# Performance work log

Measured on AMD Instinct MI355X. Metric: run time of the kernel, lower is better.

The kernel has to match this reference:

```python
import jax, jax.numpy as jnp
import numpy as np

D_MODEL = 1024
NUM_HEADS = 16
HEAD_DIM = D_MODEL // NUM_HEADS
B, S = 4, 2048


def setup_inputs() -> dict:
    key = jax.random.key(0)
    ks = jax.random.split(key, 6)
    scale = 1.0 / np.sqrt(D_MODEL)
    return {
        "q": jax.random.normal(ks[0], (B, S, D_MODEL), dtype=jnp.float32),
        "k": jax.random.normal(ks[1], (B, S, D_MODEL), dtype=jnp.float32),
        "v": jax.random.normal(ks[2], (B, S, D_MODEL), dtype=jnp.float32),
        "Wq": jax.random.normal(ks[3], (D_MODEL, D_MODEL), dtype=jnp.float32) * scale,
        "Wk": jax.random.normal(ks[4], (D_MODEL, D_MODEL), dtype=jnp.float32) * scale,
        "Wv": jax.random.normal(ks[5], (D_MODEL, D_MODEL), dtype=jnp.float32) * scale,
    }


def reference(q, k, v, Wq, Wk, Wv):
    b, s, d = q.shape
    # nn.Linear(bias=False): x @ W.T
    qp = jnp.einsum('bsd,ed->bse', q, Wq)
    kp = jnp.einsum('bsd,ed->bse', k, Wk)
    vp = jnp.einsum('bsd,ed->bse', v, Wv)
    # split heads -> (B, H, S, Dh)
    qh = qp.reshape(b, s, NUM_HEADS, HEAD_DIM).transpose(0, 2, 1, 3)
    kh = kp.reshape(b, s, NUM_HEADS, HEAD_DIM).transpose(0, 2, 1, 3)
    vh = vp.reshape(b, s, NUM_HEADS, HEAD_DIM).transpose(0, 2, 1, 3)
    scores = jnp.einsum('bhqd,bhkd->bhqk', qh, kh) / jnp.sqrt(jnp.float32(HEAD_DIM))
    attn = jax.nn.softmax(scores, axis=-1)
    att = jnp.einsum('bhqk,bhkd->bhqd', attn, vh)
    # NOTE: faithful to the source, which does a raw .view (no head transpose back)
    return att.reshape(b, s, d)
```

## Files before the change

kernel.cpp:

```cpp
#include <hip/hip_runtime.h>
#include <hip/hip_bf16.h>
#include <stdint.h>

#define D_MODEL 1024
#define NHEAD   16
#define HDIM    64
#define BATCH   4
#define SEQ     2048
#define NTOK    (BATCH*SEQ)

typedef __bf16          b16x8 __attribute__((ext_vector_type(8)));
typedef unsigned short  u16x8 __attribute__((ext_vector_type(8)));
typedef unsigned short  u16x4 __attribute__((ext_vector_type(4)));
typedef float           f32x4 __attribute__((ext_vector_type(4)));

__device__ __forceinline__ unsigned short f2b(float f) {
  union { float f; uint32_t u; } c; c.f = f;
  return (unsigned short)((c.u + 0x7FFFu + ((c.u >> 16) & 1u)) >> 16);
}

__device__ __forceinline__ uint32_t cvtpk(float lo, float hi) {
  uint32_t r;
  asm("v_cvt_pk_bf16_f32 %0, %1, %2" : "=v"(r) : "v"(lo), "v"(hi));
  return r;
}

__device__ __forceinline__ b16x8 cv8(f32x4 a, f32x4 b) {
  b16x8 r;
#pragma unroll
  for (int i = 0; i < 4; i++) { r[i] = (__bf16)a[i]; r[i + 4] = (__bf16)b[i]; }
  return r;
}

__device__ __forceinline__ void glds16(const void* g, void* l) {
  __builtin_amdgcn_global_load_lds(
      (const __attribute__((address_space(1))) unsigned int*)g,
      (__attribute__((address_space(3))) unsigned int*)l, 16, 0, 0);
}

__global__ __launch_bounds__(256, 8)
void wpack_kernel(const float* __restrict__ Wq, const float* __restrict__ Wk,
                  const float* __restrict__ Wv, unsigned short* __restrict__ wsp) {
  int bid = blockIdx.x;
  int which = bid >> 8;
  int tn = (bid >> 5) & 7;
  int kt = bid & 31;
  const float* W = (which == 0) ? Wq : ((which == 1) ? Wk : Wv);
  int t = threadIdx.x;
  int r = t >> 1;
  int sw0 = (t & 1) * 2;
  char* dst = (char*)wsp + (size_t)bid * 8192 + t * 32;
  const float* src = W + (size_t)(tn * 128 + r) * D_MODEL + kt * 32;
#pragma unroll
  for (int i = 0; i < 2; i++) {
    int s = (sw0 + i) ^ ((r >> 1) & 3);
    f32x4 a = *(const f32x4*)(src + s * 8);
    f32x4 b = *(const f32x4*)(src + s * 8 + 4);
    u16x8 pk;
#pragma unroll
    for (int j = 0; j < 4; j++) { pk[j] = f2b(a[j]); pk[j + 4] = f2b(b[j]); }
    *(u16x8*)(dst + i * 16) = pk;
  }
}

__global__ __launch_bounds__(256, 3)
void proj_gemm_f32a(const float* __restrict__ q, const float* __restrict__ k,
                    const float* __restrict__ v, const unsigned short* __restrict__ wsp,
                    unsigned short* __restrict__ qp, unsigned short* __restrict__ kp,
                    unsigned short* __restrict__ vt) {
  __shared__ __align__(16) char lds[2][24576];

  int bid = blockIdx.x;
  int swz = (bid & 7) * 192 + (bid >> 3);
  int which = swz >> 9;
  int rr = swz & 511;
  int tm = rr >> 3, tn = rr & 7;

  const float* X = (which == 0) ? q : ((which == 1) ? k : v);
  const char* Bpack = (const char*)wsp + (size_t)((which * 8 + tn) * 32) * 8192;

  int tid  = threadIdx.x;
  int lane = tid & 63;
  int w    = tid >> 6;
  int g    = lane >> 4;
  int c    = lane & 15;
  int chi  = c & 7;
  int wr   = (w >> 1) * 64;
  int wc   = (w & 1) * 64;

  f32x4 acc[4][4];
#pragma unroll
  for (int m = 0; m < 4; m++)
#pragma unroll
    for (int n = 0; n < 4; n++) acc[m][n] = (f32x4){0.f, 0.f, 0.f, 0.f};

  int arowl = lane >> 3;
  int aswz  = ((lane & 7) ^ arowl) << 4;
  const char* Asrc = (const char*)(X + (size_t)(tm * 128 + w * 32 + arowl) * D_MODEL) + aswz;
  const char* Bsrc = Bpack + w * 2048 + lane * 16;

  int aoff0 = (wr + c) * 128 + ((2 * g    ^ chi) << 4);
  int aoff1 = (wr + c) * 128 + (((2*g+1) ^ chi) << 4);
  int rboff = 16384 + (wc + c) * 64 + ((g ^ ((c >> 1) & 3)) << 4);

#pragma unroll
  for (int i = 0; i < 4; i++)
    glds16(Asrc + (size_t)i * 8 * D_MODEL * 4, lds[0] + w * 4096 + i * 1024);
  glds16(Bsrc,        lds[0] + 16384 + w * 2048);
  glds16(Bsrc + 1024, lds[0] + 16384 + w * 2048 + 1024);

  for (int kt = 0; kt < 32; kt++) {
    __syncthreads();
    if (kt < 31) {
      char* nb = lds[(kt + 1) & 1];
#pragma unroll
      for (int i = 0; i < 4; i++)
        glds16(Asrc + (size_t)i * 8 * D_MODEL * 4 + (kt + 1) * 128, nb + w * 4096 + i * 1024);
      glds16(Bsrc + (size_t)(kt + 1) * 8192,        nb + 16384 + w * 2048);
      glds16(Bsrc + (size_t)(kt + 1) * 8192 + 1024, nb + 16384 + w * 2048 + 1024);
    }
    const char* buf = lds[kt & 1];
    b16x8 af[4];
    u16x8 bf[4];
#pragma unroll
    for (int m = 0; m < 4; m++) {
      f32x4 a0 = *(const f32x4*)(buf + aoff0 + m * 2048);
      f32x4 a1 = *(const f32x4*)(buf + aoff1 + m * 2048);
      af[m] = cv8(a0, a1);
    }
#pragma unroll
    for (int n = 0; n < 4; n++)
      bf[n] = *(const u16x8*)(buf + rboff + n * 1024);
#pragma unroll
    for (int m = 0; m < 4; m++)
#pragma unroll
      for (int n = 0; n < 4; n++)
        acc[m][n] = __builtin_amdgcn_mfma_f32_16x16x32_bf16(
            af[m], __builtin_bit_cast(b16x8, bf[n]), acc[m][n], 0, 0, 0);
  }

  int cbase = tn * 128 + wc;
  int rbase = tm * 128 + wr;
  if (which < 2) {
    unsigned short* OutP = (which == 0) ? qp : kp;
    float scale = (which == 0) ? 0.18033688f : 1.0f;
#pragma unroll
    for (int m = 0; m < 4; m++)
#pragma unroll
      for (int n = 0; n < 4; n++) {
        int e = cbase + n * 16 + c;
        int h = e >> 6, dh = e & 63;
#pragma unroll
        for (int j = 0; j < 4; j++) {
          int i = rbase + m * 16 + g * 4 + j;
          int b = i >> 11, s = i & 2047;
          OutP[(((size_t)(b * NHEAD + h)) * SEQ + s) * HDIM + dh] =
              f2b(acc[m][n][j] * scale);
        }
      }
  } else {
#pragma unroll
    for (int m = 0; m < 4; m++)
#pragma unroll
      for (int n = 0; n < 4; n++) {
        int e = cbase + n * 16 + c;
        int h = e >> 6, dh = e & 63;
        int i0 = rbase + m * 16 + g * 4;
        int b = i0 >> 11, s0 = i0 & 2047;
        u16x4 pk;
#pragma unroll
        for (int j = 0; j < 4; j++) pk[j] = f2b(acc[m][n][j]);
        *(u16x4*)&vt[(((size_t)(b * NHEAD + h)) * HDIM + dh) * SEQ + s0] = pk;
      }
  }
}

#define KVB 64
__global__ __launch_bounds__(256, 4)
void attn_kernel(const unsigned short* __restrict__ qp,
                 const unsigned short* __restrict__ kp,
                 const unsigned short* __restrict__ vt,
                 float* __restrict__ out) {
  __shared__ __align__(16) char lds[2][16384];

  int bid = blockIdx.x;
  int swz = (bid & 7) * 128 + (bid >> 3);
  int bh = swz >> 4;
  int qb = swz & 15;

  int tid  = threadIdx.x;
  int lane = tid & 63;
  int w    = tid >> 6;
  int g    = lane >> 4;
  int c    = lane & 15;
  int chi  = c & 7;

  const unsigned short* Kg = kp + (size_t)bh * SEQ * HDIM;
  const unsigned short* Vg = vt + (size_t)bh * HDIM * SEQ;

  int q0 = qb * 128 + w * 32;
  u16x8 qf[2][2];
#pragma unroll
  for (int qg = 0; qg < 2; qg++)
#pragma unroll
    for (int h = 0; h < 2; h++)
      qf[qg][h] = *(const u16x8*)&qp[((size_t)bh * SEQ + q0 + qg * 16 + c) * HDIM + h * 32 + g * 8];

  f32x4 o[4][2];
#pragma unroll
  for (int d = 0; d < 4; d++)
#pragma unroll
    for (int qg = 0; qg < 2; qg++) o[d][qg] = (f32x4){0.f, 0.f, 0.f, 0.f};
  f32x4 lacc[2];
  lacc[0] = (f32x4){0.f, 0.f, 0.f, 0.f};
  lacc[1] = (f32x4){0.f, 0.f, 0.f, 0.f};

  const u16x8 ones = {0x3F80, 0x3F80, 0x3F80, 0x3F80, 0x3F80, 0x3F80, 0x3F80, 0x3F80};

  int koffA = c * 128 + ((g * 16) ^ (chi << 4));
  int koffB = c * 128 + (((64 + g * 16)) ^ (chi << 4));
  int voff[2][2];
#pragma unroll
  for (int w2 = 0; w2 < 2; w2++) {
    int b0 = w2 * 64 + g * 8;
    voff[w2][0] = 8192 + c * 128 + ((((b0      >> 4) ^ chi) << 4) + (b0 & 15));
    voff[w2][1] = 8192 + c * 128 + (((((b0+32) >> 4) ^ chi) << 4) + (b0 & 15));
  }

  int srow   = lane >> 3;
  int schunk = ((lane & 7) ^ srow) * 8;
  const unsigned short* KgL = Kg + (size_t)(w * 16 + srow) * HDIM + schunk;
  const unsigned short* VgL = Vg + (size_t)(w * 16 + srow) * SEQ + schunk;

  glds16(KgL,           lds[0] + w * 2048);
  glds16(KgL + 8 * HDIM, lds[0] + w * 2048 + 1024);
  glds16(VgL,           lds[0] + 8192 + w * 2048);
  glds16(VgL + 8 * SEQ,  lds[0] + 8192 + w * 2048 + 1024);

  for (int t = 0; t < SEQ / KVB; t++) {
    __syncthreads();
    if (t < SEQ / KVB - 1) {
      KgL += KVB * HDIM;
      VgL += KVB;
      char* nb = lds[(t + 1) & 1];
      glds16(KgL,            nb + w * 2048);
      glds16(KgL + 8 * HDIM, nb + w * 2048 + 1024);
      glds16(VgL,            nb + 8192 + w * 2048);
      glds16(VgL + 8 * SEQ,  nb + 8192 + w * 2048 + 1024);
    }
    const char* cur = lds[t & 1];

    f32x4 sf[4][2];
    __builtin_amdgcn_s_setprio(1);
#pragma unroll
    for (int st = 0; st < 4; st++) {
      u16x8 kf0 = *(const u16x8*)(cur + koffA + st * 2048);
      u16x8 kf1 = *(const u16x8*)(cur + koffB + st * 2048);
#pragma unroll
      for (int qg = 0; qg < 2; qg++) {
        sf[st][qg] = __builtin_amdgcn_mfma_f32_16x16x32_bf16(
            __builtin_bit_cast(b16x8, kf0), __builtin_bit_cast(b16x8, qf[qg][0]),
            (f32x4){0.f, 0.f, 0.f, 0.f}, 0, 0, 0);
        sf[st][qg] = __builtin_amdgcn_mfma_f32_16x16x32_bf16(
            __builtin_bit_cast(b16x8, kf1), __builtin_bit_cast(b16x8, qf[qg][1]),
            sf[st][qg], 0, 0, 0);
      }
    }
    __builtin_amdgcn_s_setprio(0);

    union { uint32_t u[4]; u16x8 v; } pb[2][2];
#pragma unroll
    for (int qg = 0; qg < 2; qg++) {
      float p[4][4];
#pragma unroll
      for (int st = 0; st < 4; st++)
#pragma unroll
        for (int j = 0; j < 4; j++) p[st][j] = exp2f(sf[st][qg][j]);
#pragma unroll
      for (int w2 = 0; w2 < 2; w2++) {
        pb[w2][qg].u[0] = cvtpk(p[2*w2][0],   p[2*w2][1]);
        pb[w2][qg].u[1] = cvtpk(p[2*w2][2],   p[2*w2][3]);
        pb[w2][qg].u[2] = cvtpk(p[2*w2+1][0], p[2*w2+1][1]);
        pb[w2][qg].u[3] = cvtpk(p[2*w2+1][2], p[2*w2+1][3]);
      }
    }

    __builtin_amdgcn_s_setprio(1);
#pragma unroll
    for (int w2 = 0; w2 < 2; w2++) {
#pragma unroll
      for (int d = 0; d < 4; d++) {
        union { u16x4 h[2]; u16x8 v; } afu;
        afu.h[0] = *(const u16x4*)(cur + voff[w2][0] + d * 2048);
        afu.h[1] = *(const u16x4*)(cur + voff[w2][1] + d * 2048);
#pragma unroll
        for (int qg = 0; qg < 2; qg++)
          o[d][qg] = __builtin_amdgcn_mfma_f32_16x16x32_bf16(
              __builtin_bit_cast(b16x8, afu.v), __builtin_bit_cast(b16x8, pb[w2][qg].v),
              o[d][qg], 0, 0, 0);
      }
#pragma unroll
      for (int qg = 0; qg < 2; qg++)
        lacc[qg] = __builtin_amdgcn_mfma_f32_16x16x32_bf16(
            __builtin_bit_cast(b16x8, ones), __builtin_bit_cast(b16x8, pb[w2][qg].v),
            lacc[qg], 0, 0, 0);
    }
    __builtin_amdgcn_s_setprio(0);
  }

#pragma unroll
  for (int qg = 0; qg < 2; qg++) {
    float inv = 1.f / lacc[qg][0];
    float* orow = out + ((size_t)bh * SEQ + q0 + qg * 16 + c) * HDIM;
#pragma unroll
    for (int d = 0; d < 4; d++) {
      f32x4 val;
#pragma unroll
      for (int j = 0; j < 4; j++) val[j] = o[d][qg][j] * inv;
      *(f32x4*)(orow + d * 16 + g * 4) = val;
    }
  }
}

extern "C" void kernel_launch(void* const* d_in, const int* in_sizes, int n_in,
                              void* d_out, int out_size, void* d_ws, size_t ws_size,
                              hipStream_t stream) {
  const float* q  = (const float*)d_in[0];
  const float* k  = (const float*)d_in[1];
  const float* v  = (const float*)d_in[2];
  const float* Wq = (const float*)d_in[3];
  const float* Wk = (const float*)d_in[4];
  const float* Wv = (const float*)d_in[5];

  const size_t projBytes = (size_t)NTOK * D_MODEL * 2;
  unsigned short* qp  = (unsigned short*)d_ws;
  unsigned short* kp  = (unsigned short*)((char*)d_ws + projBytes);
  unsigned short* vt  = (unsigned short*)((char*)d_ws + 2 * projBytes);
  unsigned short* wsp = (unsigned short*)((char*)d_ws + 3 * projBytes);
  float* out = (float*)d_out;

  hipLaunchKernelGGL(wpack_kernel, dim3(768), dim3(256), 0, stream,
                     Wq, Wk, Wv, wsp);
  hipLaunchKernelGGL(proj_gemm_f32a, dim3(1536), dim3(256), 0, stream,
                     q, k, v, wsp, qp, kp, vt);
  hipLaunchKernelGGL(attn_kernel, dim3(1024), dim3(256), 0, stream,
                     qp, kp, vt, out);
}
```

Measured before the change: 173.0 us.

## Triple-buffer projection GEMM loads with explicit vmcnt waits

Converts the projection GEMM's LDS double buffer into a three-stage ring buffer that prefetches two k-tiles ahead. It waits with explicit s_waitcnt vmcnt counts plus a raw barrier instead of __syncthreads. The goal is to hide more global-load latency behind the MFMA work. In exchange, LDS use grows to 72KB per block and launch bounds drop from 3 to 2 blocks per CU, which lowers occupancy.

```diff
diff --git a/kernel.cpp b/kernel.cpp
--- a/kernel.cpp
+++ b/kernel.cpp
@@ -63,12 +63,12 @@
   }
 }
 
-__global__ __launch_bounds__(256, 3)
+__global__ __launch_bounds__(256, 2)
 void proj_gemm_f32a(const float* __restrict__ q, const float* __restrict__ k,
                     const float* __restrict__ v, const unsigned short* __restrict__ wsp,
                     unsigned short* __restrict__ qp, unsigned short* __restrict__ kp,
                     unsigned short* __restrict__ vt) {
-  __shared__ __align__(16) char lds[2][24576];
+  __shared__ __align__(16) char lds[3][24576];
 
   int bid = blockIdx.x;
   int swz = (bid & 7) * 192 + (bid >> 3);
@@ -103,23 +103,31 @@
   int aoff1 = (wr + c) * 128 + (((2*g+1) ^ chi) << 4);
   int rboff = 16384 + (wc + c) * 64 + ((g ^ ((c >> 1) & 3)) << 4);
 
-#pragma unroll
-  for (int i = 0; i < 4; i++)
-    glds16(Asrc + (size_t)i * 8 * D_MODEL * 4, lds[0] + w * 4096 + i * 1024);
-  glds16(Bsrc,        lds[0] + 16384 + w * 2048);
-  glds16(Bsrc + 1024, lds[0] + 16384 + w * 2048 + 1024);
+  char* b0 = lds[0];
+  char* b1 = lds[1];
+  char* b2 = lds[2];
+
+#define STAGE(p, kt)                                                               \
+  do {                                                                             \
+    glds16(Asrc + (size_t)0 * 8 * D_MODEL * 4 + (kt) * 128, (p) + w * 4096 + 0 * 1024); \
+    glds16(Asrc + (size_t)1 * 8 * D_MODEL * 4 + (kt) * 128, (p) + w * 4096 + 1 * 1024); \
+    glds16(Asrc + (size_t)2 * 8 * D_MODEL * 4 + (kt) * 128, (p) + w * 4096 + 2 * 1024); \
+    glds16(Asrc + (size_t)3 * 8 * D_MODEL * 4 + (kt) * 128, (p) + w * 4096 + 3 * 1024); \
+    glds16(Bsrc + (size_t)(kt) * 8192,        (p) + 16384 + w * 2048);              \
+    glds16(Bsrc + (size_t)(kt) * 8192 + 1024, (p) + 16384 + w * 2048 + 1024);       \
+  } while (0)
+
+  STAGE(b0, 0);
+  STAGE(b1, 1);
 
   for (int kt = 0; kt < 32; kt++) {
-    __syncthreads();
-    if (kt < 31) {
-      char* nb = lds[(kt + 1) & 1];
-#pragma unroll
-      for (int i = 0; i < 4; i++)
-        glds16(Asrc + (size_t)i * 8 * D_MODEL * 4 + (kt + 1) * 128, nb + w * 4096 + i * 1024);
-      glds16(Bsrc + (size_t)(kt + 1) * 8192,        nb + 16384 + w * 2048);
-      glds16(Bsrc + (size_t)(kt + 1) * 8192 + 1024, nb + 16384 + w * 2048 + 1024);
-    }
-    const char* buf = lds[kt & 1];
+    if (kt < 31) asm volatile("s_waitcnt vmcnt(6)" ::: "memory");
+    else         asm volatile("s_waitcnt vmcnt(0)" ::: "memory");
+    __builtin_amdgcn_s_barrier();
+    __builtin_amdgcn_sched_barrier(0);
+    if (kt < 30) STAGE(b2, kt + 2);
+
+    const char* buf = b0;
     b16x8 af[4];
     u16x8 bf[4];
 #pragma unroll
@@ -137,7 +145,10 @@
       for (int n = 0; n < 4; n++)
         acc[m][n] = __builtin_amdgcn_mfma_f32_16x16x32_bf16(
             af[m], __builtin_bit_cast(b16x8, bf[n]), acc[m][n], 0, 0, 0);
-  }
+
+    char* t = b0; b0 = b1; b1 = b2; b2 = t;
+  }
+#undef STAGE
 
   int cbase = tn * 128 + wc;
   int rbase = tm * 128 + wr;
@@ -232,9 +243,9 @@
   const unsigned short* KgL = Kg + (size_t)(w * 16 + srow) * HDIM + schunk;
   const unsigned short* VgL = Vg + (size_t)(w * 16 + srow) * SEQ + schunk;
 
-  glds16(KgL,           lds[0] + w * 2048);
+  glds16(KgL,            lds[0] + w * 2048);
   glds16(KgL + 8 * HDIM, lds[0] + w * 2048 + 1024);
-  glds16(VgL,           lds[0] + 8192 + w * 2048);
+  glds16(VgL,            lds[0] + 8192 + w * 2048);
   glds16(VgL + 8 * SEQ,  lds[0] + 8192 + w * 2048 + 1024);
 
   for (int t = 0; t < SEQ / KVB; t++) {
```

Result: slower. 176.7 us (+2.2%).
